# Performance work log

Hardware: AMD Instinct MI355X
Metric: run time of the kernel (lower is better)

The kernel has to match this reference:

```python
import jax, jax.numpy as jnp
import numpy as np
import math

# Zernike (n, m) pairs for max_rank=3, m>=0, (n-m) even -> 6 invariants
PAIRS = [(0, 0), (1, 1), (2, 0), (2, 2), (3, 1), (3, 3)]
NUM_INV = len(PAIRS)
NUM_RANKS = 3          # max_rank + 1 = 2 + 1
CH_PER_RANK = 32
BN_EPS = 1e-5


def _radial(n, m, rho):
    """Zernike radial polynomial R_nm(rho) for the fixed pair set."""
    r2 = rho * rho
    if (n, m) == (0, 0):
        return jnp.ones_like(rho)
    if (n, m) == (1, 1):
        return rho
    if (n, m) == (2, 0):
        return 2.0 * r2 - 1.0
    if (n, m) == (2, 2):
        return r2
    if (n, m) == (3, 1):
        return (3.0 * r2 - 2.0) * rho
    if (n, m) == (3, 3):
        return r2 * rho
    raise ValueError((n, m))


def _zernike_pool(f):
    """f: (N, C, H, W) -> (N, NUM_INV, C).
    Center-of-mass shifted Zernike moment magnitudes, mean-pooled over space."""
    N, C, H, W = f.shape
    lin = jnp.linspace(-1.0, 1.0, H, dtype=f.dtype)
    Y, X = jnp.meshgrid(lin, lin, indexing='ij')   # (H, W)
    eps = 1e-6
    m00 = jnp.sum(f, axis=(-2, -1), keepdims=True)
    cx = jnp.sum(f * X, axis=(-2, -1), keepdims=True) / (m00 + eps)
    cy = jnp.sum(f * Y, axis=(-2, -1), keepdims=True) / (m00 + eps)
    Xs = X - cx                                    # (N, C, H, W)
    Ys = Y - cy
    rho = jnp.sqrt(Xs * Xs + Ys * Ys + 1e-12)
    theta = jnp.arctan2(Ys, Xs)
    mask = (rho <= 1.0).astype(f.dtype)            # unit-disk support
    fm = f * mask
    outs = []
    for n, m in PAIRS:
        R = _radial(n, m, rho)
        ang = m * theta
        re = jnp.mean(fm * R * jnp.cos(ang), axis=(-2, -1))
        im = -jnp.mean(fm * R * jnp.sin(ang), axis=(-2, -1))
        scale = (n + 1) / math.pi
        outs.append(scale * jnp.sqrt(re * re + im * im + 1e-12))
    return jnp.stack(outs, axis=1)                 # (N, NUM_INV, C)


def setup_inputs() -> dict:
    key = jax.random.key(0)
    k1, k2 = jax.random.split(key)
    B, H, W = 1024, 16, 16
    C_total = NUM_RANKS * CH_PER_RANK              # 96
    feats = NUM_INV * NUM_RANKS * CH_PER_RANK      # 576
    x = jax.random.normal(k1, (B, H, W, C_total), dtype=jnp.float32)
    gamma = jnp.ones((feats,), dtype=jnp.float32)
    beta = jnp.zeros((feats,), dtype=jnp.float32)
    W_lin = jax.random.normal(k2, (10, feats), dtype=jnp.float32) * 0.05
    b_lin = jnp.zeros((10,), dtype=jnp.float32)
    return {"x": x, "gamma": gamma, "beta": beta, "W_lin": W_lin, "b_lin": b_lin}


def reference(x, gamma, beta, W_lin, b_lin):
    B, H, W, Ct = x.shape
    # unflatten last dim -> (B, H, W, ranks, cpr), permute each rank slice to NCHW
    xr = x.reshape(B, H, W, NUM_RANKS, CH_PER_RANK)
    xr = jnp.transpose(xr, (0, 3, 4, 1, 2)).reshape(B * NUM_RANKS, CH_PER_RANK, H, W)
    pooled = _zernike_pool(xr)                     # (B*ranks, ninv, cpr)
    pooled = pooled.reshape(B, NUM_RANKS * NUM_INV * CH_PER_RANK)  # rank-major flatten
    # BatchNorm1d, training-mode batch statistics (biased var)
    mu = jnp.mean(pooled, axis=0)
    var = jnp.var(pooled, axis=0)
    z = (pooled - mu) / jnp.sqrt(var + BN_EPS) * gamma + beta
    return z @ W_lin.T + b_lin                     # (B, 10)
```

## Files before the change

### kernel.cpp

```cpp
#include <hip/hip_runtime.h>
#include <math.h>

#define PI_F 3.14159265358979323846f
typedef float floatx4 __attribute__((ext_vector_type(4)));

template <int CTRL>
__device__ __forceinline__ float dpp_addf(float v) {
  int p = __builtin_amdgcn_update_dpp(0, __float_as_int(v), CTRL, 0xF, 0xF, true);
  return v + __int_as_float(p);
}
__device__ __forceinline__ float red8(float v) {
  v = dpp_addf<0xB1>(v);
  v = dpp_addf<0x4E>(v);
  v = dpp_addf<0x104>(v);
  return v;
}
__device__ __forceinline__ float red16(float v) {
  v = dpp_addf<0xB1>(v);
  v = dpp_addf<0x4E>(v);
  v = dpp_addf<0x124>(v);
  v = dpp_addf<0x128>(v);
  return v;
}
__device__ __forceinline__ float red64(float v) {
  v = red16(v);
  v += __shfl_xor(v, 16);
  v += __shfl_xor(v, 32);
  return v;
}

__global__ __launch_bounds__(256) void zpool_kernel(const float* __restrict__ x,
                                                    float* __restrict__ pooled) {
  const int blk = blockIdx.x;
  const int b = blk / 3;
  const int rank = blk - b * 3;
  const floatx4* __restrict__ src4 =
      reinterpret_cast<const floatx4*>(x) + (size_t)b * 6144 + rank * 8;

  const int t = threadIdx.x;
  const int lane = t & 63;
  const int w = t >> 6;
  const int cq = lane >> 3;
  const int s = lane & 7;
  const int xcol = (8 * w + s) & 15;
  const int hoff = w >> 1;
  const float X = -1.0f + (float)xcol * (2.0f / 15.0f);

  __shared__ float p1[4][8][12];
  __shared__ float cxy[8][8];
  __shared__ float p2[4][8][40];

  floatx4 f[8];
#pragma unroll
  for (int i = 0; i < 8; ++i)
    f[i] = src4[(32 * i + 8 * w + s) * 24 + cq];

  floatx4 s0v = {0, 0, 0, 0}, syv = {0, 0, 0, 0};
#pragma unroll
  for (int i = 0; i < 8; ++i) {
    const float Y = -1.0f + (float)(2 * i + hoff) * (2.0f / 15.0f);
    s0v += f[i];
    syv += f[i] * Y;
  }
  floatx4 sxv = s0v * X;
#pragma unroll
  for (int c = 0; c < 4; ++c) {
    s0v[c] = red8(s0v[c]);
    sxv[c] = red8(sxv[c]);
    syv[c] = red8(syv[c]);
  }
  if (s == 0) {
#pragma unroll
    for (int c = 0; c < 4; ++c) {
      p1[w][cq][c] = s0v[c];
      p1[w][cq][4 + c] = sxv[c];
      p1[w][cq][8 + c] = syv[c];
    }
  }
  __syncthreads();
  if (t < 8) {
#pragma unroll
    for (int c = 0; c < 4; ++c) {
      float S0 = 0.0f, SX = 0.0f, SY = 0.0f;
#pragma unroll
      for (int w2 = 0; w2 < 4; ++w2) {
        S0 += p1[w2][t][c];
        SX += p1[w2][t][4 + c];
        SY += p1[w2][t][8 + c];
      }
      const float inv = 1.0f / (S0 + 1e-6f);
      cxy[t][c] = SX * inv;
      cxy[t][4 + c] = SY * inv;
    }
  }
  __syncthreads();
  floatx4 cx, cy;
#pragma unroll
  for (int c = 0; c < 4; ++c) { cx[c] = cxy[cq][c]; cy[c] = cxy[cq][4 + c]; }

  const floatx4 Xs = X - cx;
  const floatx4 Xs2 = Xs * Xs;
  const floatx4 Xs3 = Xs2 * Xs;
  const floatx4 lim = 1.0f - Xs2;

  floatx4 m0 = {0,0,0,0}, m1 = {0,0,0,0}, m2 = {0,0,0,0}, m3 = {0,0,0,0};
#pragma unroll
  for (int i = 0; i < 8; ++i) {
    const float Y = -1.0f + (float)(2 * i + hoff) * (2.0f / 15.0f);
    const floatx4 Ys = Y - cy;
    const floatx4 Ys2 = Ys * Ys;
    floatx4 g;
#pragma unroll
    for (int c = 0; c < 4; ++c) g[c] = (Ys2[c] <= lim[c]) ? f[i][c] : 0.0f;
    const floatx4 gy = g * Ys;
    m0 += g;
    m1 += gy;
    m2 += gy * Ys;
    m3 += gy * Ys2;
  }

  floatx4 S[10];
  S[0] = m0;        S[1] = Xs * m0;  S[2] = Xs2 * m0; S[3] = Xs3 * m0;
  S[4] = m1;        S[5] = Xs * m1;  S[6] = Xs2 * m1;
  S[7] = m2;        S[8] = Xs * m2;  S[9] = m3;
#pragma unroll
  for (int v = 0; v < 10; ++v)
#pragma unroll
    for (int c = 0; c < 4; ++c) S[v][c] = red8(S[v][c]);

  if (s == 0) {
#pragma unroll
    for (int v = 0; v < 10; ++v)
#pragma unroll
      for (int c = 0; c < 4; ++c) p2[w][cq][v * 4 + c] = S[v][c];
  }
  __syncthreads();

  if (t < 32) {
    const int fcq = t >> 2, comp = t & 3;
    float T[10];
#pragma unroll
    for (int v = 0; v < 10; ++v) {
      float acc = 0.0f;
#pragma unroll
      for (int w2 = 0; w2 < 4; ++w2) acc += p2[w2][fcq][v * 4 + comp];
      T[v] = acc;
    }
    const float S00 = T[0], S10 = T[1], S20 = T[2], S30 = T[3];
    const float S01 = T[4], S11 = T[5], S21 = T[6];
    const float S02 = T[7], S12 = T[8], S03 = T[9];
    const float a0 = S00;
    const float a1 = S10, b1 = S01;
    const float a2 = 2.0f * (S20 + S02) - S00;
    const float a3 = S20 - S02, b3 = 2.0f * S11;
    const float a4 = 3.0f * (S30 + S12) - 2.0f * S10;
    const float b4 = 3.0f * (S21 + S03) - 2.0f * S01;
    const float a5 = S30 - 3.0f * S12;
    const float b5 = 3.0f * S21 - S03;
    float* po = pooled + (size_t)b * 576 + rank * 192 + t;
    const float INV = 1.0f / 65536.0f;
    po[0]   = (1.0f / PI_F) * sqrtf(a0 * a0 * INV + 1e-12f);
    po[32]  = (2.0f / PI_F) * sqrtf(fmaf(a1, a1, b1 * b1) * INV + 1e-12f);
    po[64]  = (3.0f / PI_F) * sqrtf(a2 * a2 * INV + 1e-12f);
    po[96]  = (3.0f / PI_F) * sqrtf(fmaf(a3, a3, b3 * b3) * INV + 1e-12f);
    po[128] = (4.0f / PI_F) * sqrtf(fmaf(a4, a4, b4 * b4) * INV + 1e-12f);
    po[160] = (4.0f / PI_F) * sqrtf(fmaf(a5, a5, b5 * b5) * INV + 1e-12f);
  }
}

__global__ __launch_bounds__(256) void bn_stats_kernel(const float* __restrict__ pooled,
                                                       const float* __restrict__ gamma,
                                                       const float* __restrict__ beta,
                                                       float* __restrict__ a,
                                                       float* __restrict__ c) {
  const int f0 = blockIdx.x * 4;
  const int t = threadIdx.x;
  const floatx4* __restrict__ p =
      reinterpret_cast<const floatx4*>(pooled + f0);
  floatx4 s = {0, 0, 0, 0}, q = {0, 0, 0, 0};
#pragma unroll
  for (int j = 0; j < 4; ++j) {
    const floatx4 v = p[(size_t)(t + 256 * j) * 144];
    s += v;
    q += v * v;
  }
#pragma unroll
  for (int cc = 0; cc < 4; ++cc) {
    s[cc] = red64(s[cc]);
    q[cc] = red64(q[cc]);
  }
  __shared__ float ls[4][8];
  const int w = t >> 6;
  if ((t & 63) == 0) {
#pragma unroll
    for (int cc = 0; cc < 4; ++cc) { ls[w][cc] = s[cc]; ls[w][4 + cc] = q[cc]; }
  }
  __syncthreads();
  if (t < 4) {
    float S = 0.0f, Q = 0.0f;
#pragma unroll
    for (int i = 0; i < 4; ++i) { S += ls[i][t]; Q += ls[i][4 + t]; }
    const float mean = S * (1.0f / 1024.0f);
    const float var = fmaf(-mean, mean, Q * (1.0f / 1024.0f));
    const float istd = rsqrtf(var + 1e-5f);
    const float av = gamma[f0 + t] * istd;
    a[f0 + t] = av;
    c[f0 + t] = fmaf(-mean, av, beta[f0 + t]);
  }
}

__global__ __launch_bounds__(64) void head_kernel(const float* __restrict__ pooled,
                                                  const float* __restrict__ a,
                                                  const float* __restrict__ c,
                                                  const float* __restrict__ Wl,
                                                  const float* __restrict__ bl,
                                                  float* __restrict__ out) {
  const int row = blockIdx.x;
  const int lane = threadIdx.x;
  const float* pr = pooled + (size_t)row * 576;
  float acc0 = 0, acc1 = 0, acc2 = 0, acc3 = 0, acc4 = 0;
  float acc5 = 0, acc6 = 0, acc7 = 0, acc8 = 0, acc9 = 0;
#pragma unroll
  for (int j = 0; j < 9; ++j) {
    const int k = lane + 64 * j;
    const float z = fmaf(pr[k], a[k], c[k]);
    acc0 = fmaf(z, Wl[0 * 576 + k], acc0);
    acc1 = fmaf(z, Wl[1 * 576 + k], acc1);
    acc2 = fmaf(z, Wl[2 * 576 + k], acc2);
    acc3 = fmaf(z, Wl[3 * 576 + k], acc3);
    acc4 = fmaf(z, Wl[4 * 576 + k], acc4);
    acc5 = fmaf(z, Wl[5 * 576 + k], acc5);
    acc6 = fmaf(z, Wl[6 * 576 + k], acc6);
    acc7 = fmaf(z, Wl[7 * 576 + k], acc7);
    acc8 = fmaf(z, Wl[8 * 576 + k], acc8);
    acc9 = fmaf(z, Wl[9 * 576 + k], acc9);
  }
  acc0 = red64(acc0); acc1 = red64(acc1); acc2 = red64(acc2);
  acc3 = red64(acc3); acc4 = red64(acc4); acc5 = red64(acc5);
  acc6 = red64(acc6); acc7 = red64(acc7); acc8 = red64(acc8);
  acc9 = red64(acc9);
  if (lane == 0) {
    float* o = out + (size_t)row * 10;
    o[0] = acc0 + bl[0]; o[1] = acc1 + bl[1]; o[2] = acc2 + bl[2];
    o[3] = acc3 + bl[3]; o[4] = acc4 + bl[4]; o[5] = acc5 + bl[5];
    o[6] = acc6 + bl[6]; o[7] = acc7 + bl[7]; o[8] = acc8 + bl[8];
    o[9] = acc9 + bl[9];
  }
}

extern "C" void kernel_launch(void* const* d_in, const int* in_sizes, int n_in,
                              void* d_out, int out_size, void* d_ws, size_t ws_size,
                              hipStream_t stream) {
  const float* x     = (const float*)d_in[0];
  const float* gamma = (const float*)d_in[1];
  const float* beta  = (const float*)d_in[2];
  const float* Wl    = (const float*)d_in[3];
  const float* bl    = (const float*)d_in[4];
  float* out = (float*)d_out;

  float* pooled = (float*)d_ws;
  float* a = pooled + 576 * 1024;
  float* c = a + 576;

  zpool_kernel<<<3072, 256, 0, stream>>>(x, pooled);
  bn_stats_kernel<<<144, 256, 0, stream>>>(pooled, gamma, beta, a, c);
  head_kernel<<<1024, 64, 0, stream>>>(pooled, a, c, Wl, bl, out);
}
```

Measured before the change: 34.09 us.

## Fuse BatchNorm statistics into pooling kernel via atomics, drop stats kernel

Removes the separate bn_stats kernel. The pooling kernel now atomically accumulates per-feature sum and sum-of-squares into a stats buffer, and the head kernel computes mean, variance and the scale/shift itself. This is meant to save a kernel launch and a full re-read of the pooled matrix. In exchange it adds a memset, 1024-way atomic contention per feature address, a non-deterministic summation order, and redundant per-block stats math in the head kernel.

```diff
diff --git a/kernel.cpp b/kernel.cpp
--- a/kernel.cpp
+++ b/kernel.cpp
@@ -30,7 +30,8 @@
 }
 
 __global__ __launch_bounds__(256) void zpool_kernel(const float* __restrict__ x,
-                                                    float* __restrict__ pooled) {
+                                                    float* __restrict__ pooled,
+                                                    float* __restrict__ stats) {
   const int blk = blockIdx.x;
   const int b = blk / 3;
   const int rank = blk - b * 3;
@@ -157,73 +158,53 @@
     const float b4 = 3.0f * (S21 + S03) - 2.0f * S01;
     const float a5 = S30 - 3.0f * S12;
     const float b5 = 3.0f * S21 - S03;
-    float* po = pooled + (size_t)b * 576 + rank * 192 + t;
+    const int fbase = rank * 192 + t;
+    float* po = pooled + (size_t)b * 576 + fbase;
     const float INV = 1.0f / 65536.0f;
-    po[0]   = (1.0f / PI_F) * sqrtf(a0 * a0 * INV + 1e-12f);
-    po[32]  = (2.0f / PI_F) * sqrtf(fmaf(a1, a1, b1 * b1) * INV + 1e-12f);
-    po[64]  = (3.0f / PI_F) * sqrtf(a2 * a2 * INV + 1e-12f);
-    po[96]  = (3.0f / PI_F) * sqrtf(fmaf(a3, a3, b3 * b3) * INV + 1e-12f);
-    po[128] = (4.0f / PI_F) * sqrtf(fmaf(a4, a4, b4 * b4) * INV + 1e-12f);
-    po[160] = (4.0f / PI_F) * sqrtf(fmaf(a5, a5, b5 * b5) * INV + 1e-12f);
-  }
-}
-
-__global__ __launch_bounds__(256) void bn_stats_kernel(const float* __restrict__ pooled,
-                                                       const float* __restrict__ gamma,
-                                                       const float* __restrict__ beta,
-                                                       float* __restrict__ a,
-                                                       float* __restrict__ c) {
-  const int f0 = blockIdx.x * 4;
-  const int t = threadIdx.x;
-  const floatx4* __restrict__ p =
-      reinterpret_cast<const floatx4*>(pooled + f0);
-  floatx4 s = {0, 0, 0, 0}, q = {0, 0, 0, 0};
-#pragma unroll
-  for (int j = 0; j < 4; ++j) {
-    const floatx4 v = p[(size_t)(t + 256 * j) * 144];
-    s += v;
-    q += v * v;
-  }
-#pragma unroll
-  for (int cc = 0; cc < 4; ++cc) {
-    s[cc] = red64(s[cc]);
-    q[cc] = red64(q[cc]);
-  }
-  __shared__ float ls[4][8];
-  const int w = t >> 6;
-  if ((t & 63) == 0) {
-#pragma unroll
-    for (int cc = 0; cc < 4; ++cc) { ls[w][cc] = s[cc]; ls[w][4 + cc] = q[cc]; }
-  }
-  __syncthreads();
-  if (t < 4) {
-    float S = 0.0f, Q = 0.0f;
-#pragma unroll
-    for (int i = 0; i < 4; ++i) { S += ls[i][t]; Q += ls[i][4 + t]; }
-    const float mean = S * (1.0f / 1024.0f);
-    const float var = fmaf(-mean, mean, Q * (1.0f / 1024.0f));
-    const float istd = rsqrtf(var + 1e-5f);
-    const float av = gamma[f0 + t] * istd;
-    a[f0 + t] = av;
-    c[f0 + t] = fmaf(-mean, av, beta[f0 + t]);
+    float vals[6];
+    vals[0] = (1.0f / PI_F) * sqrtf(a0 * a0 * INV + 1e-12f);
+    vals[1] = (2.0f / PI_F) * sqrtf(fmaf(a1, a1, b1 * b1) * INV + 1e-12f);
+    vals[2] = (3.0f / PI_F) * sqrtf(a2 * a2 * INV + 1e-12f);
+    vals[3] = (3.0f / PI_F) * sqrtf(fmaf(a3, a3, b3 * b3) * INV + 1e-12f);
+    vals[4] = (4.0f / PI_F) * sqrtf(fmaf(a4, a4, b4 * b4) * INV + 1e-12f);
+    vals[5] = (4.0f / PI_F) * sqrtf(fmaf(a5, a5, b5 * b5) * INV + 1e-12f);
+#pragma unroll
+    for (int v = 0; v < 6; ++v) {
+      po[v * 32] = vals[v];
+      atomicAdd(&stats[fbase + v * 32], vals[v]);
+      atomicAdd(&stats[576 + fbase + v * 32], vals[v] * vals[v]);
+    }
   }
 }
 
 __global__ __launch_bounds__(64) void head_kernel(const float* __restrict__ pooled,
-                                                  const float* __restrict__ a,
-                                                  const float* __restrict__ c,
+                                                  const float* __restrict__ stats,
+                                                  const float* __restrict__ gamma,
+                                                  const float* __restrict__ beta,
                                                   const float* __restrict__ Wl,
                                                   const float* __restrict__ bl,
                                                   float* __restrict__ out) {
   const int row = blockIdx.x;
   const int lane = threadIdx.x;
   const float* pr = pooled + (size_t)row * 576;
+
+  float av[9], cv[9];
+#pragma unroll
+  for (int j = 0; j < 9; ++j) {
+    const int k = lane + 64 * j;
+    const float mean = stats[k] * (1.0f / 1024.0f);
+    const float var = fmaf(-mean, mean, stats[576 + k] * (1.0f / 1024.0f));
+    const float istd = rsqrtf(var + 1e-5f);
+    av[j] = gamma[k] * istd;
+    cv[j] = fmaf(-mean, av[j], beta[k]);
+  }
+
   float acc0 = 0, acc1 = 0, acc2 = 0, acc3 = 0, acc4 = 0;
   float acc5 = 0, acc6 = 0, acc7 = 0, acc8 = 0, acc9 = 0;
 #pragma unroll
   for (int j = 0; j < 9; ++j) {
     const int k = lane + 64 * j;
-    const float z = fmaf(pr[k], a[k], c[k]);
+    const float z = fmaf(pr[k], av[j], cv[j]);
     acc0 = fmaf(z, Wl[0 * 576 + k], acc0);
     acc1 = fmaf(z, Wl[1 * 576 + k], acc1);
     acc2 = fmaf(z, Wl[2 * 576 + k], acc2);
@@ -259,10 +240,9 @@
   float* out = (float*)d_out;
 
   float* pooled = (float*)d_ws;
-  float* a = pooled + 576 * 1024;
-  float* c = a + 576;
-
-  zpool_kernel<<<3072, 256, 0, stream>>>(x, pooled);
-  bn_stats_kernel<<<144, 256, 0, stream>>>(pooled, gamma, beta, a, c);
-  head_kernel<<<1024, 64, 0, stream>>>(pooled, a, c, Wl, bl, out);
-}
+  float* stats = pooled + 576 * 1024;
+
+  hipMemsetAsync(stats, 0, 1152 * sizeof(float), stream);
+  zpool_kernel<<<3072, 256, 0, stream>>>(x, pooled, stats);
+  head_kernel<<<1024, 64, 0, stream>>>(pooled, stats, gamma, beta, Wl, bl, out);
+}
```

Result: slower. 47.04 us (+38.0%).
